# Kernel optimization log

Measured on AMD Instinct MI355X. Metric: run time of the kernel, lower is better.

## Reference

```python
import jax, jax.numpy as jnp
import numpy as np

B, SQ, SK, D, H, DH = 4, 1024, 1024, 1024, 16, 64

def setup_inputs() -> dict:
    key = jax.random.key(0)
    ks = jax.random.split(key, 7)
    s = 0.02
    return {
        "input_ids": jax.random.normal(ks[0], (B, SQ, D), jnp.float32),
        "encoder_output": jax.random.normal(ks[1], (B, SK, D), jnp.float32),
        "position_bias": jax.random.normal(ks[2], (1, H, SQ, SK), jnp.float32),
        "Wq": jax.random.normal(ks[3], (D, H * DH), jnp.float32) * s,
        "Wk": jax.random.normal(ks[4], (D, H * DH), jnp.float32) * s,
        "Wv": jax.random.normal(ks[5], (D, H * DH), jnp.float32) * s,
        "Wo": jax.random.normal(ks[6], (H * DH, D), jnp.float32) * s,
    }

def reference(input_ids, encoder_output, position_bias, Wq, Wk, Wv, Wo):
    # bias-free projections (nn.Linear(..., bias=False))
    q = (input_ids @ Wq).reshape(B, SQ, H, DH).transpose(0, 2, 1, 3)      # [B,H,Sq,dh]
    k = (encoder_output @ Wk).reshape(B, SK, H, DH).transpose(0, 2, 1, 3)  # [B,H,Sk,dh]
    v = (encoder_output @ Wv).reshape(B, SK, H, DH).transpose(0, 2, 1, 3)  # [B,H,Sk,dh]
    # T5-style attention: NO 1/sqrt(dh) scaling, additive position bias
    scores = jnp.einsum("bhqd,bhkd->bhqk", q, k) + position_bias          # [B,H,Sq,Sk]
    attn = jax.nn.softmax(scores, axis=-1)
    ctx = jnp.einsum("bhqk,bhkd->bhqd", attn, v)                          # [B,H,Sq,dh]
    ctx = ctx.transpose(0, 2, 1, 3).reshape(B, SQ, H * DH)
    return ctx @ Wo                                                        # [B,Sq,D]
```

## Files before the change

kernel.cpp:

```cpp
#include <hip/hip_runtime.h>

typedef _Float16 f16;
typedef _Float16 f16x4 __attribute__((ext_vector_type(4)));
typedef _Float16 f16x8 __attribute__((ext_vector_type(8)));
typedef float f32x4 __attribute__((ext_vector_type(4)));

#define LOADLDS16(gp, lp)                                                     \
  __builtin_amdgcn_global_load_lds(                                           \
      (const __attribute__((address_space(1))) void*)(gp),                    \
      (__attribute__((address_space(3))) void*)(lp), 16, 0, 0)

__global__ __launch_bounds__(256) void k_cast2(const float* __restrict__ a,
                                               const float* __restrict__ b,
                                               f16* __restrict__ ya,
                                               f16* __restrict__ yb) {
  int i = blockIdx.x * 256 + threadIdx.x;
  const float* x;
  f16* y;
  if (i < 1048576) {
    x = a; y = ya;
  } else {
    x = b; y = yb; i -= 1048576;
  }
  float4 v = reinterpret_cast<const float4*>(x)[i];
  f16x4 o;
  o[0] = (f16)v.x; o[1] = (f16)v.y; o[2] = (f16)v.z; o[3] = (f16)v.w;
  reinterpret_cast<f16x4*>(y)[i] = o;
}

__global__ __launch_bounds__(256) void k_castw_t(
    const float* __restrict__ w0, const float* __restrict__ w1,
    const float* __restrict__ w2, const float* __restrict__ w3,
    f16* __restrict__ o0, f16* __restrict__ o1, f16* __restrict__ o2,
    f16* __restrict__ o3) {
  const float* W;
  f16* O;
  switch (blockIdx.z) {
    case 0: W = w0; O = o0; break;
    case 1: W = w1; O = o1; break;
    case 2: W = w2; O = o2; break;
    default: W = w3; O = o3; break;
  }
  __shared__ f16 T[64][72];
  const int tid = threadIdx.x;
  const int r0 = blockIdx.y * 64, c0 = blockIdx.x * 64;
#pragma unroll
  for (int i = 0; i < 4; ++i) {
    int c = i * 256 + tid;
    int row = c >> 4, col = (c & 15) * 4;
    float4 v = *reinterpret_cast<const float4*>(W + (size_t)(r0 + row) * 1024 + c0 + col);
    T[col + 0][row] = (f16)v.x;
    T[col + 1][row] = (f16)v.y;
    T[col + 2][row] = (f16)v.z;
    T[col + 3][row] = (f16)v.w;
  }
  __syncthreads();
#pragma unroll
  for (int i = 0; i < 2; ++i) {
    int c = i * 256 + tid;
    int cc = c >> 3, ro = (c & 7) * 8;
    f16x8 v;
#pragma unroll
    for (int j = 0; j < 8; ++j) v[j] = T[cc][ro + j];
    *reinterpret_cast<f16x8*>(O + (size_t)(c0 + cc) * 1024 + r0 + ro) = v;
  }
}

__global__ __launch_bounds__(256) void k_gemm_qkv(const f16* __restrict__ Xq,
                                                  const f16* __restrict__ Xkv,
                                                  const f16* __restrict__ Bt,
                                                  f16* __restrict__ outp) {
  __shared__ f16 As[128 * 64];
  __shared__ f16 Bs[128 * 64];
  const int tid = threadIdx.x;
  const int w = tid >> 6, l = tid & 63;
  const int lr = l & 15, lq = l >> 4;
  const int m0 = blockIdx.y * 128, n0 = blockIdx.x * 128;
  const f16* A = (n0 < 1024) ? Xq : Xkv;
  const int wr = (w >> 1) * 64, wc = (w & 1) * 64;
  const int K = 1024;
  f32x4 acc[4][4] = {};
  for (int kt = 0; kt < K; kt += 64) {
#pragma unroll
    for (int i = 0; i < 4; ++i) {
      int c = (i * 4 + w) * 64 + l;
      LOADLDS16(A + (size_t)(m0 + (c >> 3)) * K + kt + (c & 7) * 8,
                As + (size_t)(i * 4 + w) * 512);
      LOADLDS16(Bt + (size_t)(n0 + (c >> 3)) * K + kt + (c & 7) * 8,
                Bs + (size_t)(i * 4 + w) * 512);
    }
    __syncthreads();
#pragma unroll
    for (int kk = 0; kk < 2; ++kk) {
      f16x8 af[4], bf[4];
#pragma unroll
      for (int m = 0; m < 4; ++m)
        af[m] = *reinterpret_cast<const f16x8*>(As + (wr + m * 16 + lr) * 64 + kk * 32 + lq * 8);
#pragma unroll
      for (int n = 0; n < 4; ++n)
        bf[n] = *reinterpret_cast<const f16x8*>(Bs + (wc + n * 16 + lr) * 64 + kk * 32 + lq * 8);
#pragma unroll
      for (int m = 0; m < 4; ++m)
#pragma unroll
        for (int n = 0; n < 4; ++n)
          acc[m][n] = __builtin_amdgcn_mfma_f32_16x16x32_f16(af[m], bf[n], acc[m][n], 0, 0, 0);
    }
    __syncthreads();
  }
  const bool vplane = (n0 >= 2048);
#pragma unroll
  for (int m = 0; m < 4; ++m)
#pragma unroll
    for (int n = 0; n < 4; ++n) {
      int col = n0 + wc + n * 16 + lr;
      int row0 = m0 + wr + m * 16 + lq * 4;
      int b = row0 >> 10, s0 = row0 & 1023;
      int plane = col >> 10, cc = col & 1023;
      int h = cc >> 6, dh = cc & 63;
      if (vplane) {
        f16x4 v4;
#pragma unroll
        for (int r = 0; r < 4; ++r) v4[r] = (f16)acc[m][n][r];
        *reinterpret_cast<f16x4*>(
            outp + (size_t)2 * 4194304 +
            ((size_t)(b * 16 + h)) * 65536 + (size_t)dh * 1024 + s0) = v4;
      } else {
#pragma unroll
        for (int r = 0; r < 4; ++r)
          outp[(size_t)plane * 4194304 +
               (((size_t)(b * 16 + h)) * 1024 + s0 + r) * 64 + dh] =
              (f16)acc[m][n][r];
      }
    }
}

__global__ __launch_bounds__(256) void k_gemm_o(const f16* __restrict__ A,
                                                const f16* __restrict__ Bt,
                                                float* __restrict__ out, int M,
                                                int N, int K) {
  __shared__ f16 As[64 * 64];
  __shared__ f16 Bs[128 * 64];
  const int tid = threadIdx.x;
  const int w = tid >> 6, l = tid & 63;
  const int lr = l & 15, lq = l >> 4;
  const int m0 = blockIdx.y * 64, n0 = blockIdx.x * 128;
  const int wr = (w >> 1) * 32, wc = (w & 1) * 64;
  f32x4 acc[2][4] = {};
  for (int kt = 0; kt < K; kt += 64) {
#pragma unroll
    for (int i = 0; i < 2; ++i) {
      int c = (i * 4 + w) * 64 + l;
      LOADLDS16(A + (size_t)(m0 + (c >> 3)) * K + kt + (c & 7) * 8,
                As + (size_t)(i * 4 + w) * 512);
    }
#pragma unroll
    for (int i = 0; i < 4; ++i) {
      int c = (i * 4 + w) * 64 + l;
      LOADLDS16(Bt + (size_t)(n0 + (c >> 3)) * K + kt + (c & 7) * 8,
                Bs + (size_t)(i * 4 + w) * 512);
    }
    __syncthreads();
#pragma unroll
    for (int kk = 0; kk < 2; ++kk) {
      f16x8 af[2], bf[4];
#pragma unroll
      for (int m = 0; m < 2; ++m)
        af[m] = *reinterpret_cast<const f16x8*>(As + (wr + m * 16 + lr) * 64 + kk * 32 + lq * 8);
#pragma unroll
      for (int n = 0; n < 4; ++n)
        bf[n] = *reinterpret_cast<const f16x8*>(Bs + (wc + n * 16 + lr) * 64 + kk * 32 + lq * 8);
#pragma unroll
      for (int m = 0; m < 2; ++m)
#pragma unroll
        for (int n = 0; n < 4; ++n)
          acc[m][n] = __builtin_amdgcn_mfma_f32_16x16x32_f16(af[m], bf[n], acc[m][n], 0, 0, 0);
    }
    __syncthreads();
  }
#pragma unroll
  for (int m = 0; m < 2; ++m)
#pragma unroll
    for (int n = 0; n < 4; ++n)
#pragma unroll
      for (int r = 0; r < 4; ++r) {
        int row = m0 + wr + m * 16 + lq * 4 + r;
        int col = n0 + wc + n * 16 + lr;
        out[(size_t)row * N + col] = acc[m][n][r];
      }
}

__global__ __launch_bounds__(256) void k_attn(const f16* __restrict__ qb,
                                              const f16* __restrict__ kb,
                                              const f16* __restrict__ vtb,
                                              const float* __restrict__ bias,
                                              f16* __restrict__ ctx) {
  const int bid = blockIdx.x;
  const int ord = (bid & 7) * 128 + (bid >> 3);
  const int h = ord >> 6, b = (ord >> 4) & 3, qt = ord & 15;
  const int bh = b * 16 + h;
  const int q0 = qt * 64;
  const int tid = threadIdx.x, w = tid >> 6, l = tid & 63;
  const int lr = l & 15, lq = l >> 4;

  __shared__ f16 Kb[2][4096];
  __shared__ f16 Vb[2][4096];

  const f16* qp = qb + ((size_t)bh * 1024 + q0 + w * 16 + lr) * 64 + lq * 8;
  f16x8 qf0 = *reinterpret_cast<const f16x8*>(qp);
  f16x8 qf1 = *reinterpret_cast<const f16x8*>(qp + 32);

  f32x4 O[4] = {};
  float mrun = -3.0e38f, rsum = 0.f;

  const f16* kbase = kb + (size_t)bh * 65536;
  const f16* vbase = vtb + (size_t)bh * 65536;
  const float* bq = bias + ((size_t)h * 1024 + q0 + w * 16 + lr) * 1024 + lq * 4;

  auto stage = [&](int t, int nxt) {
#pragma unroll
    for (int i = 0; i < 2; ++i) {
      int c = (i * 4 + w) * 64 + l;
      int row = c >> 3, g = (c & 7) ^ (row & 7);
      LOADLDS16(kbase + (size_t)(t * 64 + row) * 64 + g * 8,
                &Kb[nxt][(i * 4 + w) * 512]);
      LOADLDS16(vbase + (size_t)row * 1024 + t * 64 + g * 8,
                &Vb[nxt][(i * 4 + w) * 512]);
    }
  };

  stage(0, 0);

#pragma unroll 1
  for (int t = 0; t < 16; ++t) {
    const int cur = t & 1;
    __builtin_amdgcn_s_barrier();
    if (t < 15) stage(t + 1, cur ^ 1);
    f32x4 bf[4];
#pragma unroll
    for (int c = 0; c < 4; ++c)
      bf[c] = *reinterpret_cast<const f32x4*>(bq + t * 64 + c * 16);
    __builtin_amdgcn_sched_barrier(0);
    if (t < 15) {
      asm volatile("s_waitcnt vmcnt(8)" ::: "memory");
    } else {
      asm volatile("s_waitcnt vmcnt(4)" ::: "memory");
    }
    __builtin_amdgcn_sched_barrier(0);

    f32x4 S[4] = {};
    __builtin_amdgcn_s_setprio(1);
#pragma unroll
    for (int c = 0; c < 4; ++c) {
      int row = c * 16 + lr;
      const f16* kbp = &Kb[cur][row * 64];
      f16x8 kf0 = *reinterpret_cast<const f16x8*>(kbp + ((lq ^ (row & 7)) * 8));
      f16x8 kf1 = *reinterpret_cast<const f16x8*>(kbp + (((4 + lq) ^ (row & 7)) * 8));
      S[c] = __builtin_amdgcn_mfma_f32_16x16x32_f16(kf0, qf0, S[c], 0, 0, 0);
      S[c] = __builtin_amdgcn_mfma_f32_16x16x32_f16(kf1, qf1, S[c], 0, 0, 0);
    }
    __builtin_amdgcn_s_setprio(0);

#pragma unroll
    for (int c = 0; c < 4; ++c)
#pragma unroll
      for (int r = 0; r < 4; ++r) S[c][r] += bf[c][r];

    float tmax = fmaxf(
        fmaxf(fmaxf(fmaxf(S[0][0], S[0][1]), fmaxf(S[0][2], S[0][3])),
              fmaxf(fmaxf(S[1][0], S[1][1]), fmaxf(S[1][2], S[1][3]))),
        fmaxf(fmaxf(fmaxf(S[2][0], S[2][1]), fmaxf(S[2][2], S[2][3])),
              fmaxf(fmaxf(S[3][0], S[3][1]), fmaxf(S[3][2], S[3][3]))));
    if (!__all(tmax <= mrun + 8.0f)) {
      tmax = fmaxf(tmax, __shfl_xor(tmax, 16, 64));
      tmax = fmaxf(tmax, __shfl_xor(tmax, 32, 64));
      float mnew = fmaxf(mrun, tmax);
      float sc = __expf(mrun - mnew);
      mrun = mnew;
      rsum *= sc;
      int sb = l & 48;
#pragma unroll
      for (int r = 0; r < 4; ++r) {
        float scO = __shfl(sc, sb | (lq * 4 + r), 64);
#pragma unroll
        for (int c = 0; c < 4; ++c) O[c][r] *= scO;
      }
    }

    f32x4 p[4];
#pragma unroll
    for (int c = 0; c < 4; ++c) {
#pragma unroll
      for (int r = 0; r < 4; ++r) p[c][r] = __expf(S[c][r] - mrun);
      rsum += (p[c][0] + p[c][1]) + (p[c][2] + p[c][3]);
    }
    f16x8 pa0, pa1;
#pragma unroll
    for (int j = 0; j < 4; ++j) {
      pa0[j] = (f16)p[0][j];
      pa0[4 + j] = (f16)p[1][j];
      pa1[j] = (f16)p[2][j];
      pa1[4 + j] = (f16)p[3][j];
    }

    __builtin_amdgcn_s_setprio(1);
#pragma unroll
    for (int c = 0; c < 4; ++c) {
      int row = c * 16 + lr;
      const f16* vbp = &Vb[cur][row * 64];
      int s8 = row & 7, sub = (lq & 1) * 4, gh = lq >> 1;
      f16x4 v0 = *reinterpret_cast<const f16x4*>(vbp + ((gh ^ s8) * 8 + sub));
      f16x4 v1 = *reinterpret_cast<const f16x4*>(vbp + (((2 + gh) ^ s8) * 8 + sub));
      f16x4 v2 = *reinterpret_cast<const f16x4*>(vbp + (((4 + gh) ^ s8) * 8 + sub));
      f16x4 v3 = *reinterpret_cast<const f16x4*>(vbp + (((6 + gh) ^ s8) * 8 + sub));
      f16x8 vf0, vf1;
#pragma unroll
      for (int j = 0; j < 4; ++j) {
        vf0[j] = v0[j];
        vf0[4 + j] = v1[j];
        vf1[j] = v2[j];
        vf1[4 + j] = v3[j];
      }
      O[c] = __builtin_amdgcn_mfma_f32_16x16x32_f16(pa0, vf0, O[c], 0, 0, 0);
      O[c] = __builtin_amdgcn_mfma_f32_16x16x32_f16(pa1, vf1, O[c], 0, 0, 0);
    }
    __builtin_amdgcn_s_setprio(0);
    __builtin_amdgcn_sched_barrier(0);
  }

  rsum += __shfl_xor(rsum, 16, 64);
  rsum += __shfl_xor(rsum, 32, 64);
  int sb = l & 48;
  float rs[4];
#pragma unroll
  for (int r = 0; r < 4; ++r) rs[r] = __shfl(rsum, sb | (lq * 4 + r), 64);

#pragma unroll
  for (int c = 0; c < 4; ++c)
#pragma unroll
    for (int r = 0; r < 4; ++r) {
      float o = O[c][r] / rs[r];
      int row = q0 + w * 16 + lq * 4 + r;
      ctx[((size_t)b * 1024 + row) * 1024 + h * 64 + c * 16 + lr] = (f16)o;
    }
}

extern "C" void kernel_launch(void* const* d_in, const int* in_sizes, int n_in,
                              void* d_out, int out_size, void* d_ws,
                              size_t ws_size, hipStream_t stream) {
  const float* input_ids = (const float*)d_in[0];
  const float* enc = (const float*)d_in[1];
  const float* bias = (const float*)d_in[2];
  const float* Wq = (const float*)d_in[3];
  const float* Wk = (const float*)d_in[4];
  const float* Wv = (const float*)d_in[5];
  const float* Wo = (const float*)d_in[6];

  char* ws = (char*)d_ws;
  const size_t MB = 1024 * 1024;
  f16* Xq  = (f16*)(ws + 0 * MB);
  f16* Xkv = (f16*)(ws + 8 * MB);
  f16* Wqt = (f16*)(ws + 16 * MB);
  f16* Wkt = (f16*)(ws + 18 * MB);
  f16* Wvt = (f16*)(ws + 20 * MB);
  f16* Wot = (f16*)(ws + 22 * MB);
  f16* qbuf = (f16*)(ws + 24 * MB);
  f16* kbuf = (f16*)(ws + 32 * MB);
  f16* vtb  = (f16*)(ws + 40 * MB);
  f16* ctxb = Xq;

  k_cast2<<<8192, 256, 0, stream>>>(input_ids, enc, Xq, Xkv);
  k_castw_t<<<dim3(16, 16, 4), 256, 0, stream>>>(Wq, Wk, Wv, Wo, Wqt, Wkt, Wvt, Wot);

  k_gemm_qkv<<<dim3(24, 32), 256, 0, stream>>>(Xq, Xkv, Wqt, qbuf);

  k_attn<<<1024, 256, 0, stream>>>(qbuf, kbuf, vtb, bias, ctxb);

  k_gemm_o<<<dim3(8, 64), 256, 0, stream>>>(ctxb, Wot, (float*)d_out, 4096, 1024, 1024);
}
```

Baseline: 137.8 us.

## Restructure attention blocks to share position-bias rows across batches per head

The attention kernel now runs 512-thread blocks over one head and 32 query rows, with 8 waves covering 4 batches times 2 query sub-tiles. The key tile shrinks from 64 to 32 and the loop runs 32 iterations. Bias loads are prefetched one step ahead in ping-pong registers, and the barrier and wait move to the end of each step. Since the bias is the same for every batch, co-scheduling the batches of a head is meant to improve cache reuse of the large fp32 bias tensor. The cost is smaller MFMA work per step, twice as many barriers, and larger per-block LDS.

```diff
diff --git a/kernel.cpp b/kernel.cpp
--- a/kernel.cpp
+++ b/kernel.cpp
@@ -189,70 +189,74 @@
       }
 }
 
-__global__ __launch_bounds__(256) void k_attn(const f16* __restrict__ qb,
+__global__ __launch_bounds__(512) void k_attn(const f16* __restrict__ qb,
                                               const f16* __restrict__ kb,
                                               const f16* __restrict__ vtb,
                                               const float* __restrict__ bias,
                                               f16* __restrict__ ctx) {
   const int bid = blockIdx.x;
-  const int ord = (bid & 7) * 128 + (bid >> 3);
-  const int h = ord >> 6, b = (ord >> 4) & 3, qt = ord & 15;
-  const int bh = b * 16 + h;
-  const int q0 = qt * 64;
+  const int ord = (bid & 7) * 64 + (bid >> 3);
+  const int h = ord >> 5, qt = ord & 31;
+  const int q0 = qt * 32;
   const int tid = threadIdx.x, w = tid >> 6, l = tid & 63;
   const int lr = l & 15, lq = l >> 4;
-
-  __shared__ f16 Kb[2][4096];
-  __shared__ f16 Vb[2][4096];
-
-  const f16* qp = qb + ((size_t)bh * 1024 + q0 + w * 16 + lr) * 64 + lq * 8;
+  const int bb = w >> 1, qs = w & 1;
+  const int bh = bb * 16 + h;
+
+  __shared__ f16 Kb[2][8192];
+  __shared__ f16 Vb[2][8192];
+
+  const f16* qp = qb + ((size_t)bh * 1024 + q0 + qs * 16 + lr) * 64 + lq * 8;
   f16x8 qf0 = *reinterpret_cast<const f16x8*>(qp);
   f16x8 qf1 = *reinterpret_cast<const f16x8*>(qp + 32);
 
   f32x4 O[4] = {};
   float mrun = -3.0e38f, rsum = 0.f;
 
-  const f16* kbase = kb + (size_t)bh * 65536;
-  const f16* vbase = vtb + (size_t)bh * 65536;
-  const float* bq = bias + ((size_t)h * 1024 + q0 + w * 16 + lr) * 1024 + lq * 4;
+  const float* bq =
+      bias + ((size_t)h * 1024 + q0 + qs * 16 + lr) * 1024 + lq * 4;
 
   auto stage = [&](int t, int nxt) {
 #pragma unroll
     for (int i = 0; i < 2; ++i) {
-      int c = (i * 4 + w) * 64 + l;
-      int row = c >> 3, g = (c & 7) ^ (row & 7);
-      LOADLDS16(kbase + (size_t)(t * 64 + row) * 64 + g * 8,
-                &Kb[nxt][(i * 4 + w) * 512]);
-      LOADLDS16(vbase + (size_t)row * 1024 + t * 64 + g * 8,
-                &Vb[nxt][(i * 4 + w) * 512]);
+      int c = i * 512 + tid;
+      int bb2 = c >> 8, cc = c & 255;
+      int bh2 = bb2 * 16 + h;
+      int kr = cc >> 3, kg = (cc & 7) ^ (kr & 7);
+      LOADLDS16(kb + (size_t)bh2 * 65536 + (size_t)(t * 32 + kr) * 64 + kg * 8,
+                &Kb[nxt][(size_t)(i * 512 + w * 64) * 8]);
+      int vr = cc >> 2, vg = (cc & 3) ^ (vr & 3);
+      LOADLDS16(vtb + (size_t)bh2 * 65536 + (size_t)vr * 1024 + t * 32 + vg * 8,
+                &Vb[nxt][(size_t)(i * 512 + w * 64) * 8]);
     }
   };
 
   stage(0, 0);
-
-#pragma unroll 1
-  for (int t = 0; t < 16; ++t) {
+  f32x4 bA[2], bB[2];
+#pragma unroll
+  for (int c = 0; c < 2; ++c) bA[c] = *reinterpret_cast<const f32x4*>(bq + c * 16);
+  asm volatile("s_waitcnt vmcnt(2)" ::: "memory");
+  __builtin_amdgcn_sched_barrier(0);
+  __builtin_amdgcn_s_barrier();
+
+  auto body = [&](int t, f32x4 (&bc)[2], f32x4 (&bn)[2]) {
     const int cur = t & 1;
-    __builtin_amdgcn_s_barrier();
-    if (t < 15) stage(t + 1, cur ^ 1);
-    f32x4 bf[4];
-#pragma unroll
-    for (int c = 0; c < 4; ++c)
-      bf[c] = *reinterpret_cast<const f32x4*>(bq + t * 64 + c * 16);
+    if (t < 31) {
+      stage(t + 1, cur ^ 1);
+      __builtin_amdgcn_sched_barrier(0);
+#pragma unroll
+      for (int c = 0; c < 2; ++c)
+        bn[c] = *reinterpret_cast<const f32x4*>(bq + (t + 1) * 32 + c * 16);
+    }
     __builtin_amdgcn_sched_barrier(0);
-    if (t < 15) {
-      asm volatile("s_waitcnt vmcnt(8)" ::: "memory");
-    } else {
-      asm volatile("s_waitcnt vmcnt(4)" ::: "memory");
-    }
-    __builtin_amdgcn_sched_barrier(0);
-
-    f32x4 S[4] = {};
+
+    const f16* Kcb = &Kb[cur][bb * 2048];
+    f32x4 S[2] = {};
     __builtin_amdgcn_s_setprio(1);
 #pragma unroll
-    for (int c = 0; c < 4; ++c) {
+    for (int c = 0; c < 2; ++c) {
       int row = c * 16 + lr;
-      const f16* kbp = &Kb[cur][row * 64];
+      const f16* kbp = Kcb + row * 64;
       f16x8 kf0 = *reinterpret_cast<const f16x8*>(kbp + ((lq ^ (row & 7)) * 8));
       f16x8 kf1 = *reinterpret_cast<const f16x8*>(kbp + (((4 + lq) ^ (row & 7)) * 8));
       S[c] = __builtin_amdgcn_mfma_f32_16x16x32_f16(kf0, qf0, S[c], 0, 0, 0);
@@ -261,15 +265,12 @@
     __builtin_amdgcn_s_setprio(0);
 
 #pragma unroll
-    for (int c = 0; c < 4; ++c)
-#pragma unroll
-      for (int r = 0; r < 4; ++r) S[c][r] += bf[c][r];
-
-    float tmax = fmaxf(
-        fmaxf(fmaxf(fmaxf(S[0][0], S[0][1]), fmaxf(S[0][2], S[0][3])),
-              fmaxf(fmaxf(S[1][0], S[1][1]), fmaxf(S[1][2], S[1][3]))),
-        fmaxf(fmaxf(fmaxf(S[2][0], S[2][1]), fmaxf(S[2][2], S[2][3])),
-              fmaxf(fmaxf(S[3][0], S[3][1]), fmaxf(S[3][2], S[3][3]))));
+    for (int c = 0; c < 2; ++c)
+#pragma unroll
+      for (int r = 0; r < 4; ++r) S[c][r] += bc[c][r];
+
+    float tmax = fmaxf(fmaxf(fmaxf(S[0][0], S[0][1]), fmaxf(S[0][2], S[0][3])),
+                       fmaxf(fmaxf(S[1][0], S[1][1]), fmaxf(S[1][2], S[1][3])));
     if (!__all(tmax <= mrun + 8.0f)) {
       tmax = fmaxf(tmax, __shfl_xor(tmax, 16, 64));
       tmax = fmaxf(tmax, __shfl_xor(tmax, 32, 64));
@@ -286,45 +287,51 @@
       }
     }
 
-    f32x4 p[4];
-#pragma unroll
-    for (int c = 0; c < 4; ++c) {
+    f32x4 p[2];
+#pragma unroll
+    for (int c = 0; c < 2; ++c) {
 #pragma unroll
       for (int r = 0; r < 4; ++r) p[c][r] = __expf(S[c][r] - mrun);
       rsum += (p[c][0] + p[c][1]) + (p[c][2] + p[c][3]);
     }
-    f16x8 pa0, pa1;
+    f16x8 pa;
 #pragma unroll
     for (int j = 0; j < 4; ++j) {
-      pa0[j] = (f16)p[0][j];
-      pa0[4 + j] = (f16)p[1][j];
-      pa1[j] = (f16)p[2][j];
-      pa1[4 + j] = (f16)p[3][j];
-    }
-
+      pa[j] = (f16)p[0][j];
+      pa[4 + j] = (f16)p[1][j];
+    }
+
+    const f16* Vcb = &Vb[cur][bb * 2048];
     __builtin_amdgcn_s_setprio(1);
 #pragma unroll
     for (int c = 0; c < 4; ++c) {
       int row = c * 16 + lr;
-      const f16* vbp = &Vb[cur][row * 64];
-      int s8 = row & 7, sub = (lq & 1) * 4, gh = lq >> 1;
-      f16x4 v0 = *reinterpret_cast<const f16x4*>(vbp + ((gh ^ s8) * 8 + sub));
-      f16x4 v1 = *reinterpret_cast<const f16x4*>(vbp + (((2 + gh) ^ s8) * 8 + sub));
-      f16x4 v2 = *reinterpret_cast<const f16x4*>(vbp + (((4 + gh) ^ s8) * 8 + sub));
-      f16x4 v3 = *reinterpret_cast<const f16x4*>(vbp + (((6 + gh) ^ s8) * 8 + sub));
-      f16x8 vf0, vf1;
+      const f16* vbp = Vcb + row * 32;
+      int s4 = row & 3, sub = (lq & 1) * 4, gh = lq >> 1;
+      f16x4 v0 = *reinterpret_cast<const f16x4*>(vbp + ((gh ^ s4) * 8 + sub));
+      f16x4 v1 = *reinterpret_cast<const f16x4*>(vbp + (((2 + gh) ^ s4) * 8 + sub));
+      f16x8 vf;
 #pragma unroll
       for (int j = 0; j < 4; ++j) {
-        vf0[j] = v0[j];
-        vf0[4 + j] = v1[j];
-        vf1[j] = v2[j];
-        vf1[4 + j] = v3[j];
+        vf[j] = v0[j];
+        vf[4 + j] = v1[j];
       }
-      O[c] = __builtin_amdgcn_mfma_f32_16x16x32_f16(pa0, vf0, O[c], 0, 0, 0);
-      O[c] = __builtin_amdgcn_mfma_f32_16x16x32_f16(pa1, vf1, O[c], 0, 0, 0);
+      O[c] = __builtin_amdgcn_mfma_f32_16x16x32_f16(pa, vf, O[c], 0, 0, 0);
     }
     __builtin_amdgcn_s_setprio(0);
     __builtin_amdgcn_sched_barrier(0);
+
+    if (t < 31) {
+      asm volatile("s_waitcnt vmcnt(2)" ::: "memory");
+      __builtin_amdgcn_sched_barrier(0);
+      __builtin_amdgcn_s_barrier();
+    }
+  };
+
+#pragma unroll 1
+  for (int ith = 0; ith < 16; ++ith) {
+    body(2 * ith, bA, bB);
+    body(2 * ith + 1, bB, bA);
   }
 
   rsum += __shfl_xor(rsum, 16, 64);
@@ -339,8 +346,8 @@
 #pragma unroll
     for (int r = 0; r < 4; ++r) {
       float o = O[c][r] / rs[r];
-      int row = q0 + w * 16 + lq * 4 + r;
-      ctx[((size_t)b * 1024 + row) * 1024 + h * 64 + c * 16 + lr] = (f16)o;
+      int row = q0 + qs * 16 + lq * 4 + r;
+      ctx[((size_t)bb * 1024 + row) * 1024 + h * 64 + c * 16 + lr] = (f16)o;
     }
 }
 
@@ -373,7 +380,7 @@
 
   k_gemm_qkv<<<dim3(24, 32), 256, 0, stream>>>(Xq, Xkv, Wqt, qbuf);
 
-  k_attn<<<1024, 256, 0, stream>>>(qbuf, kbuf, vtb, bias, ctxb);
+  k_attn<<<512, 512, 0, stream>>>(qbuf, kbuf, vtb, bias, ctxb);
 
   k_gemm_o<<<dim3(8, 64), 256, 0, stream>>>(ctxb, Wot, (float*)d_out, 4096, 1024, 1024);
 }
```

After: 151.8 us. +10.1%, slower.
